# Performance work log

Hardware: AMD Instinct MI355X
Metric: run time of the kernel (lower is better)

## Reference

```python
import jax, jax.numpy as jnp
import numpy as np

BETA = 0.25
ORTHO_L = 10.0


def setup_inputs() -> dict:
    key = jax.random.key(0)
    kx, kw = jax.random.split(key)
    x = jax.random.normal(kx, (64, 256, 32, 32), dtype=jnp.float32)
    # torch init: uniform(-1/K, 1/D); use normal-scale-free uniform for parity of math
    K, D = 1024, 256
    weight = jax.random.uniform(kw, (K, D), dtype=jnp.float32,
                                minval=-1.0 / K, maxval=1.0 / D)
    return {"x": x, "weight": weight}


def reference(x, weight):
    B, C, H, W = x.shape
    K, D = weight.shape
    xp = jnp.transpose(x, (0, 2, 3, 1))            # [B,H,W,D]
    flat = xp.reshape(-1, D)                        # [N,D], N=B*H*W
    d = (jnp.sum(flat * flat, axis=1, keepdims=True)
         + jnp.sum(weight * weight, axis=1)
         - 2.0 * flat @ weight.T)                   # [N,K]
    idx = jnp.argmin(d, axis=1)                     # [N]
    # one_hot @ weight == row gather
    x_q = weight[idx].reshape(xp.shape)             # [B,H,W,D]
    # commitment / codebook loss with stop-gradient semantics of .detach()
    sg = jax.lax.stop_gradient
    loss = jnp.mean((sg(x_q) - xp) ** 2) + BETA * jnp.mean((x_q - sg(xp)) ** 2)
    # orthogonal regularizer on detached codebook (torch uses .data)
    w_d = sg(weight)
    w_n = w_d / jnp.linalg.norm(w_d, axis=-1, keepdims=True)
    s = w_n @ w_n.T                                 # [K,K]
    loss = loss + ORTHO_L * (jnp.linalg.norm(s - jnp.eye(K, dtype=s.dtype)) / (K ** 2))
    # straight-through estimator
    x_q_st = xp + sg(x_q - xp)
    out = jnp.transpose(x_q_st, (0, 3, 1, 2))       # [B,C,H,W]
    return out, loss, idx.reshape(B, -1)
```

## Files before the change

kernel.cpp:

```cpp
#include <hip/hip_runtime.h>
#include <math.h>

#define D 256
#define K 1024
#define N_PTS 65536
#define BETA 0.25f
#define ORTHO_L 10.0f

#define OUT_ELEMS 16777216
#define LOSS_OFF 16777216
#define IDX_OFF  16777217

#define WS_SSE_VQ    0
#define WS_SSE_ORTHO 1
#define WS_B         2
#define WS_NORM      (2 + 1024)

__global__ __launch_bounds__(64) void codes_kernel(const float* __restrict__ w,
                                                   float* __restrict__ ws) {
    int k = blockIdx.x;
    int lane = threadIdx.x;
    float4 v = *(const float4*)(w + (size_t)k * D + lane * 4);
    float s = v.x * v.x + v.y * v.y + v.z * v.z + v.w * v.w;
    for (int m = 32; m; m >>= 1) s += __shfl_xor(s, m, 64);
    if (lane == 0) {
        ws[WS_B + k] = s;
        ws[WS_NORM + k] = sqrtf(s);
    }
}

#define MT 32
#define NT 128
#define DC 32

__global__ __launch_bounds__(256) void argmin_kernel(const float* __restrict__ x,
                                                     const float* __restrict__ w,
                                                     const float* __restrict__ ws,
                                                     float* __restrict__ out_idx) {
    __shared__ float Xs[D][MT];
    __shared__ float Ws[DC][NT];
    __shared__ float Apart[8][MT];
    __shared__ float Ash[MT];

    int tid = threadIdx.x;
    int tx = tid & 31;
    int ty = tid >> 5;

    int n0 = blockIdx.x * MT;
    int b  = n0 >> 10;
    int hw0 = n0 & 1023;

    const float* xb = x + (size_t)b * (D * 1024) + hw0;
    {
        int p = tid & 31;
        int cq = tid >> 5;
        for (int c0 = 0; c0 < D; c0 += 8) {
            int c = c0 + cq;
            Xs[c][p] = xb[(size_t)c * 1024 + p];
        }
    }
    __syncthreads();

    {
        int p = tid & 31;
        int q = tid >> 5;
        float s = 0.f;
        #pragma unroll
        for (int d = 0; d < 32; ++d) {
            float v = Xs[q * 32 + d][p];
            s += v * v;
        }
        Apart[q][p] = s;
    }
    __syncthreads();
    if (tid < MT) {
        float s = 0.f;
        #pragma unroll
        for (int q = 0; q < 8; ++q) s += Apart[q][tid];
        Ash[tid] = s;
    }
    __syncthreads();

    float bestv[4];
    int   besti[4];
    #pragma unroll
    for (int i = 0; i < 4; ++i) { bestv[i] = 3.4e38f; besti[i] = 0; }

    for (int kc = 0; kc < K / NT; ++kc) {
        float acc[4][4];
        #pragma unroll
        for (int i = 0; i < 4; ++i)
            #pragma unroll
            for (int j = 0; j < 4; ++j) acc[i][j] = 0.f;

        for (int dc = 0; dc < D / DC; ++dc) {
            int r = tid >> 1;
            int dbase = (tid & 1) << 4;
            const float* wr = w + (size_t)(kc * NT + r) * D + dc * DC + dbase;
            float4 a0 = *(const float4*)(wr + 0);
            float4 a1 = *(const float4*)(wr + 4);
            float4 a2 = *(const float4*)(wr + 8);
            float4 a3 = *(const float4*)(wr + 12);

            __syncthreads();
            Ws[dbase + 0][r] = a0.x;  Ws[dbase + 1][r] = a0.y;
            Ws[dbase + 2][r] = a0.z;  Ws[dbase + 3][r] = a0.w;
            Ws[dbase + 4][r] = a1.x;  Ws[dbase + 5][r] = a1.y;
            Ws[dbase + 6][r] = a1.z;  Ws[dbase + 7][r] = a1.w;
            Ws[dbase + 8][r] = a2.x;  Ws[dbase + 9][r] = a2.y;
            Ws[dbase +10][r] = a2.z;  Ws[dbase +11][r] = a2.w;
            Ws[dbase +12][r] = a3.x;  Ws[dbase +13][r] = a3.y;
            Ws[dbase +14][r] = a3.z;  Ws[dbase +15][r] = a3.w;
            __syncthreads();

            #pragma unroll 4
            for (int d = 0; d < DC; ++d) {
                float4 xv = *(const float4*)&Xs[dc * DC + d][ty * 4];
                float4 wv = *(const float4*)&Ws[d][tx * 4];
                acc[0][0] += xv.x * wv.x;  acc[0][1] += xv.x * wv.y;
                acc[0][2] += xv.x * wv.z;  acc[0][3] += xv.x * wv.w;
                acc[1][0] += xv.y * wv.x;  acc[1][1] += xv.y * wv.y;
                acc[1][2] += xv.y * wv.z;  acc[1][3] += xv.y * wv.w;
                acc[2][0] += xv.z * wv.x;  acc[2][1] += xv.z * wv.y;
                acc[2][2] += xv.z * wv.z;  acc[2][3] += xv.z * wv.w;
                acc[3][0] += xv.w * wv.x;  acc[3][1] += xv.w * wv.y;
                acc[3][2] += xv.w * wv.z;  acc[3][3] += xv.w * wv.w;
            }
        }

        int p0 = ty * 4;
        int kb = kc * NT + tx * 4;
        #pragma unroll
        for (int i = 0; i < 4; ++i) {
            float a = Ash[p0 + i];
            #pragma unroll
            for (int j = 0; j < 4; ++j) {
                float t  = a + ws[WS_B + kb + j];
                float dv = t - 2.0f * acc[i][j];
                if (dv < bestv[i]) { bestv[i] = dv; besti[i] = kb + j; }
            }
        }
    }

    #pragma unroll
    for (int i = 0; i < 4; ++i) {
        float v = bestv[i];
        int ix = besti[i];
        for (int m = 16; m; m >>= 1) {
            float v2 = __shfl_xor(v, m, 64);
            int   i2 = __shfl_xor(ix, m, 64);
            if (v2 < v || (v2 == v && i2 < ix)) { v = v2; ix = i2; }
        }
        if (tx == 0) out_idx[n0 + ty * 4 + i] = (float)ix;
    }
}

__global__ __launch_bounds__(256) void gather_kernel(const float* __restrict__ x,
                                                     const float* __restrict__ w,
                                                     const float* __restrict__ idxf,
                                                     float* __restrict__ out,
                                                     float* __restrict__ ws) {
    __shared__ float red[256];
    int tid = threadIdx.x;
    size_t t0 = (size_t)blockIdx.x * 256 + tid;
    const size_t total4 = OUT_ELEMS / 4;
    const size_t stride = (size_t)2048 * 256;

    float sse = 0.f;
    for (size_t e4 = t0; e4 < total4; e4 += stride) {
        size_t e = e4 * 4;
        int b  = (int)(e >> 18);
        int c  = (int)((e >> 10) & 255);
        int hw = (int)(e & 1023);
        int n  = (b << 10) + hw;

        float4 xv = *(const float4*)(x + e);
        int k0 = (int)idxf[n + 0];
        int k1 = (int)idxf[n + 1];
        int k2 = (int)idxf[n + 2];
        int k3 = (int)idxf[n + 3];
        float w0 = w[(size_t)k0 * D + c];
        float w1 = w[(size_t)k1 * D + c];
        float w2 = w[(size_t)k2 * D + c];
        float w3 = w[(size_t)k3 * D + c];
        float d0 = w0 - xv.x, d1 = w1 - xv.y, d2 = w2 - xv.z, d3 = w3 - xv.w;
        float4 ov;
        ov.x = xv.x + d0;  ov.y = xv.y + d1;
        ov.z = xv.z + d2;  ov.w = xv.w + d3;
        *(float4*)(out + e) = ov;
        sse += d0 * d0 + d1 * d1 + d2 * d2 + d3 * d3;
    }

    red[tid] = sse;
    __syncthreads();
    for (int s = 128; s > 0; s >>= 1) {
        if (tid < s) red[tid] += red[tid + s];
        __syncthreads();
    }
    if (tid == 0) atomicAdd(ws + WS_SSE_VQ, red[0]);
}

__global__ __launch_bounds__(256) void ortho_kernel(const float* __restrict__ w,
                                                    float* __restrict__ ws) {
    __shared__ float wi[D];
    __shared__ float wsum[4];
    int i = blockIdx.x;
    int tid = threadIdx.x;
    int lane = tid & 63;
    int wid = tid >> 6;

    if (tid < 64)
        *(float4*)&wi[tid * 4] = *(const float4*)(w + (size_t)i * D + tid * 4);
    __syncthreads();

    float inv_i = 1.0f / ws[WS_NORM + i];
    float acc = 0.f;
    for (int j = wid; j < K; j += 4) {
        float4 a = *(const float4*)(w + (size_t)j * D + lane * 4);
        float4 bq = *(const float4*)&wi[lane * 4];
        float s = a.x * bq.x + a.y * bq.y + a.z * bq.z + a.w * bq.w;
        for (int m = 32; m; m >>= 1) s += __shfl_xor(s, m, 64);
        float sij = s * inv_i * (1.0f / ws[WS_NORM + j]);
        float t = sij - (j == i ? 1.0f : 0.0f);
        acc += t * t;
    }
    if (lane == 0) wsum[wid] = acc;
    __syncthreads();
    if (tid == 0)
        atomicAdd(ws + WS_SSE_ORTHO, wsum[0] + wsum[1] + wsum[2] + wsum[3]);
}

__global__ void finalize_kernel(const float* __restrict__ ws, float* __restrict__ out) {
    float loss = (1.0f + BETA) * ws[WS_SSE_VQ] / (float)OUT_ELEMS
               + ORTHO_L * sqrtf(ws[WS_SSE_ORTHO]) / ((float)K * (float)K);
    out[LOSS_OFF] = loss;
}

extern "C" void kernel_launch(void* const* d_in, const int* in_sizes, int n_in,
                              void* d_out, int out_size, void* d_ws, size_t ws_size,
                              hipStream_t stream) {
    const float* x = (const float*)d_in[0];
    const float* w = (const float*)d_in[1];
    float* out = (float*)d_out;
    float* ws  = (float*)d_ws;

    hipMemsetAsync(d_ws, 0, 2 * sizeof(float), stream);
    codes_kernel<<<K, 64, 0, stream>>>(w, ws);
    argmin_kernel<<<N_PTS / MT, 256, 0, stream>>>(x, w, ws, out + IDX_OFF);
    ortho_kernel<<<K, 256, 0, stream>>>(w, ws);
    gather_kernel<<<2048, 256, 0, stream>>>(x, w, out + IDX_OFF, out, ws);
    finalize_kernel<<<1, 1, 0, stream>>>(ws, out);
}
```

Measured before the change: 735.7 us.

## Restructure argmin GEMM to 8x16 register tiles over full codebook with prefetch

The argmin kernel now has each thread accumulate an 8-point by 16-code tile, so one block covers all 1024 codes in a single pass over D instead of looping over code chunks. Codebook slices of 8 dims are register-prefetched for the next chunk while the current one is computed, and code norms are staged in shared memory. This is meant to raise FMA-to-LDS ratio and remove the repeated outer loop and global norm reads. In exchange it uses 128 accumulators per thread, which raises register pressure despite launch bounds of 2 blocks, and it puts a larger Ws tile in LDS.

```diff
diff --git a/kernel.cpp b/kernel.cpp
--- a/kernel.cpp
+++ b/kernel.cpp
@@ -29,22 +29,24 @@
     }
 }
 
-#define MT 32
-#define NT 128
-#define DC 32
-
-__global__ __launch_bounds__(256) void argmin_kernel(const float* __restrict__ x,
-                                                     const float* __restrict__ w,
-                                                     const float* __restrict__ ws,
-                                                     float* __restrict__ out_idx) {
+#define MT  32
+#define DCH 8
+#define NCHUNK (D / DCH)
+
+__global__ __launch_bounds__(256, 2) void argmin_kernel(const float* __restrict__ x,
+                                                        const float* __restrict__ w,
+                                                        const float* __restrict__ wsb,
+                                                        float* __restrict__ out_idx) {
     __shared__ float Xs[D][MT];
-    __shared__ float Ws[DC][NT];
+    __shared__ float Ws[DCH][K];
+    __shared__ float Bs[K];
     __shared__ float Apart[8][MT];
     __shared__ float Ash[MT];
 
     int tid = threadIdx.x;
-    int tx = tid & 31;
-    int ty = tid >> 5;
+    int tx = tid & 63;
+    int py = tid >> 6;
+    int p0 = py * 8;
 
     int n0 = blockIdx.x * MT;
     int b  = n0 >> 10;
@@ -59,6 +61,7 @@
             Xs[c][p] = xb[(size_t)c * 1024 + p];
         }
     }
+    *(float4*)&Bs[tid * 4] = *(const float4*)&wsb[WS_B + tid * 4];
     __syncthreads();
 
     {
@@ -79,79 +82,78 @@
         for (int q = 0; q < 8; ++q) s += Apart[q][tid];
         Ash[tid] = s;
     }
-    __syncthreads();
-
-    float bestv[4];
-    int   besti[4];
+
+    float acc[8][16];
     #pragma unroll
-    for (int i = 0; i < 4; ++i) { bestv[i] = 3.4e38f; besti[i] = 0; }
-
-    for (int kc = 0; kc < K / NT; ++kc) {
-        float acc[4][4];
-        #pragma unroll
-        for (int i = 0; i < 4; ++i)
+    for (int i = 0; i < 8; ++i)
+        #pragma unroll
+        for (int j = 0; j < 16; ++j) acc[i][j] = 0.f;
+
+    int cstage = tid >> 1;
+    int dh     = (tid & 1) * 4;
+
+    float4 sreg[8];
+    #pragma unroll
+    for (int p = 0; p < 8; ++p)
+        sreg[p] = *(const float4*)(w + (size_t)(p * 128 + cstage) * D + 0 * DCH + dh);
+
+    for (int dc = 0; dc < NCHUNK; ++dc) {
+        __syncthreads();
+        #pragma unroll
+        for (int p = 0; p < 8; ++p) {
+            int c = p * 128 + cstage;
+            Ws[dh + 0][c] = sreg[p].x;
+            Ws[dh + 1][c] = sreg[p].y;
+            Ws[dh + 2][c] = sreg[p].z;
+            Ws[dh + 3][c] = sreg[p].w;
+        }
+        __syncthreads();
+        if (dc + 1 < NCHUNK) {
             #pragma unroll
-            for (int j = 0; j < 4; ++j) acc[i][j] = 0.f;
-
-        for (int dc = 0; dc < D / DC; ++dc) {
-            int r = tid >> 1;
-            int dbase = (tid & 1) << 4;
-            const float* wr = w + (size_t)(kc * NT + r) * D + dc * DC + dbase;
-            float4 a0 = *(const float4*)(wr + 0);
-            float4 a1 = *(const float4*)(wr + 4);
-            float4 a2 = *(const float4*)(wr + 8);
-            float4 a3 = *(const float4*)(wr + 12);
-
-            __syncthreads();
-            Ws[dbase + 0][r] = a0.x;  Ws[dbase + 1][r] = a0.y;
-            Ws[dbase + 2][r] = a0.z;  Ws[dbase + 3][r] = a0.w;
-            Ws[dbase + 4][r] = a1.x;  Ws[dbase + 5][r] = a1.y;
-            Ws[dbase + 6][r] = a1.z;  Ws[dbase + 7][r] = a1.w;
-            Ws[dbase + 8][r] = a2.x;  Ws[dbase + 9][r] = a2.y;
-            Ws[dbase +10][r] = a2.z;  Ws[dbase +11][r] = a2.w;
-            Ws[dbase +12][r] = a3.x;  Ws[dbase +13][r] = a3.y;
-            Ws[dbase +14][r] = a3.z;  Ws[dbase +15][r] = a3.w;
-            __syncthreads();
-
-            #pragma unroll 4
-            for (int d = 0; d < DC; ++d) {
-                float4 xv = *(const float4*)&Xs[dc * DC + d][ty * 4];
-                float4 wv = *(const float4*)&Ws[d][tx * 4];
-                acc[0][0] += xv.x * wv.x;  acc[0][1] += xv.x * wv.y;
-                acc[0][2] += xv.x * wv.z;  acc[0][3] += xv.x * wv.w;
-                acc[1][0] += xv.y * wv.x;  acc[1][1] += xv.y * wv.y;
-                acc[1][2] += xv.y * wv.z;  acc[1][3] += xv.y * wv.w;
-                acc[2][0] += xv.z * wv.x;  acc[2][1] += xv.z * wv.y;
-                acc[2][2] += xv.z * wv.z;  acc[2][3] += xv.z * wv.w;
-                acc[3][0] += xv.w * wv.x;  acc[3][1] += xv.w * wv.y;
-                acc[3][2] += xv.w * wv.z;  acc[3][3] += xv.w * wv.w;
+            for (int p = 0; p < 8; ++p)
+                sreg[p] = *(const float4*)(w + (size_t)(p * 128 + cstage) * D + (dc + 1) * DCH + dh);
+        }
+
+        #pragma unroll
+        for (int d = 0; d < DCH; ++d) {
+            float4 x0 = *(const float4*)&Xs[dc * DCH + d][p0];
+            float4 x1 = *(const float4*)&Xs[dc * DCH + d][p0 + 4];
+            float xr[8] = {x0.x, x0.y, x0.z, x0.w, x1.x, x1.y, x1.z, x1.w};
+            #pragma unroll
+            for (int m = 0; m < 4; ++m) {
+                float4 wv = *(const float4*)&Ws[d][tx * 4 + m * 256];
+                #pragma unroll
+                for (int i = 0; i < 8; ++i) {
+                    acc[i][m * 4 + 0] += xr[i] * wv.x;
+                    acc[i][m * 4 + 1] += xr[i] * wv.y;
+                    acc[i][m * 4 + 2] += xr[i] * wv.z;
+                    acc[i][m * 4 + 3] += xr[i] * wv.w;
+                }
             }
         }
-
-        int p0 = ty * 4;
-        int kb = kc * NT + tx * 4;
-        #pragma unroll
-        for (int i = 0; i < 4; ++i) {
-            float a = Ash[p0 + i];
+    }
+
+    #pragma unroll
+    for (int i = 0; i < 8; ++i) {
+        float a = Ash[p0 + i];
+        float bv = 3.4e38f;
+        int   bi = 0;
+        #pragma unroll
+        for (int m = 0; m < 4; ++m) {
             #pragma unroll
             for (int j = 0; j < 4; ++j) {
-                float t  = a + ws[WS_B + kb + j];
-                float dv = t - 2.0f * acc[i][j];
-                if (dv < bestv[i]) { bestv[i] = dv; besti[i] = kb + j; }
+                int k = tx * 4 + m * 256 + j;
+                float t  = a + Bs[k];
+                float dv = t - 2.0f * acc[i][m * 4 + j];
+                if (dv < bv) { bv = dv; bi = k; }
             }
         }
-    }
-
-    #pragma unroll
-    for (int i = 0; i < 4; ++i) {
-        float v = bestv[i];
-        int ix = besti[i];
-        for (int m = 16; m; m >>= 1) {
-            float v2 = __shfl_xor(v, m, 64);
-            int   i2 = __shfl_xor(ix, m, 64);
-            if (v2 < v || (v2 == v && i2 < ix)) { v = v2; ix = i2; }
-        }
-        if (tx == 0) out_idx[n0 + ty * 4 + i] = (float)ix;
+        for (int mm = 32; mm; mm >>= 1) {
+            float v2 = __shfl_xor(bv, mm, 64);
+            int   i2 = __shfl_xor(bi, mm, 64);
+            if (v2 < bv || (v2 == bv && i2 < bi)) { bv = v2; bi = i2; }
+        }
+        if (tx == 0) out_idx[n0 + p0 + i] = (float)bi;
     }
 }
 
```

Result: slower. 1.184 ms (+60.9%).
